# Optimization experiments

Measured on AMD Instinct MI355X. Metric: run time of the kernel, lower is better.

Reference implementation:

```python
import jax, jax.numpy as jnp
import numpy as np

K = 3  # kernel_size

def setup_inputs() -> dict:
    key = jax.random.key(0)
    k1, k2 = jax.random.split(key)
    inputs = jax.random.normal(k1, (16, 96, 96, 64), dtype=jnp.float32)
    # Dense weights for each of the K*K taps; Dense input dim == cout (conv output channels)
    W = jax.random.normal(k2, (K, K, 128, 128), dtype=jnp.float32) * 0.05
    return {"inputs": inputs, "W": W}

def reference(inputs, W):
    # inputs: [B,H,Wd,Cin], W: [K,K,cout,cout]
    B, H, Wd, Cin = inputs.shape
    pad = (K - 1) // 2  # TF 'same' padding, stride 1, odd kernel
    # One-hot conv kernel ones((cin,cout)) at tap (x,y): every output channel equals the
    # channel-sum of the zero-padded input shifted by (x-pad, y-pad).
    s = inputs.sum(axis=-1)  # [B,H,Wd]
    sp = jnp.pad(s, ((0, 0), (pad, pad), (pad, pad)))  # [B,H+2p,Wd+2p]
    # shifted[x,y,b,i,j] = sp[b, i+x, j+y]
    shifted = jnp.stack([
        jnp.stack([sp[:, x:x + H, y:y + Wd] for y in range(K)], axis=0)
        for x in range(K)], axis=0)  # [K,K,B,H,Wd]
    # Dense(no bias) on a constant-across-channels vector: out_o = s * sum_c W[c,o]
    wsum = W.sum(axis=2)  # [K,K,cout]
    out = shifted[..., None] * wsum[:, :, None, None, None, :]  # [K,K,B,H,Wd,cout]
    return out
```

## Files before the change

kernel.cpp:

```cpp
#include <hip/hip_runtime.h>

#define BQ   16
#define HH   96
#define WWD  96
#define CIN  64
#define COUT 128
#define KK   3
#define NPIX (BQ * HH * WWD)

typedef float f32x4 __attribute__((ext_vector_type(4)));

__global__ __launch_bounds__(256) void k_prep(const float* __restrict__ in,
                                              const float* __restrict__ W,
                                              float* __restrict__ s,
                                              float* __restrict__ wsum) {
    int t = threadIdx.x;
    if (blockIdx.x < KK * KK) {
        int tap = blockIdx.x;
        int o    = t & (COUT - 1);
        int half = t >> 7;
        const float* base = W + (size_t)tap * COUT * COUT + (size_t)half * 64 * COUT + o;
        float acc = 0.f;
#pragma unroll 8
        for (int c = 0; c < 64; ++c) acc += base[(size_t)c * COUT];
        __shared__ float red[256];
        red[t] = acc;
        __syncthreads();
        if (t < COUT) wsum[tap * COUT + t] = red[t] + red[t + COUT];
        return;
    }
    int pb = blockIdx.x - KK * KK;
    int g  = t & 15;
#pragma unroll
    for (int it = 0; it < 16; ++it) {
        int pixel = pb * 256 + it * 16 + (t >> 4);
        f32x4 v = __builtin_nontemporal_load(
            (const f32x4*)(in + (size_t)pixel * CIN) + g);
        float acc = (v.x + v.y) + (v.z + v.w);
        acc += __shfl_xor(acc, 1);
        acc += __shfl_xor(acc, 2);
        acc += __shfl_xor(acc, 4);
        acc += __shfl_xor(acc, 8);
        if (g == 0) s[pixel] = acc;
    }
}

__global__ __launch_bounds__(256) void k_main(const float* __restrict__ s,
                                              const float* __restrict__ wsum,
                                              float* __restrict__ out) {
    int bid = blockIdx.x;
    int tap = bid / (BQ * HH);
    int rem = bid - tap * (BQ * HH);
    int b   = rem / HH;
    int i   = rem - b * HH;
    int x   = tap / 3, y = tap - x * 3;

    int t  = threadIdx.x;
    int ob = (t & 31) * 4;
    int jt = t >> 5;

    f32x4 w = *(const f32x4*)(wsum + tap * COUT + ob);

    int ii = i + x - 1;
    bool rowok = (unsigned)ii < (unsigned)HH;
    const float* srow = s + ((size_t)b * HH + (rowok ? ii : 0)) * WWD;
    float* orow = out + (size_t)bid * (WWD * COUT) + ob;

#pragma unroll
    for (int it = 0; it < WWD / 8; ++it) {
        int j  = it * 8 + jt;
        int jj = j + y - 1;
        float sv = (rowok && (unsigned)jj < (unsigned)WWD) ? srow[jj] : 0.f;
        f32x4 v = { sv * w.x, sv * w.y, sv * w.z, sv * w.w };
        __builtin_nontemporal_store(v, (f32x4*)(orow + (size_t)j * COUT));
    }
}

extern "C" void kernel_launch(void* const* d_in, const int* in_sizes, int n_in,
                              void* d_out, int out_size, void* d_ws, size_t ws_size,
                              hipStream_t stream) {
    const float* in = (const float*)d_in[0];
    const float* W  = (const float*)d_in[1];
    float* out  = (float*)d_out;
    float* s    = (float*)d_ws;
    float* wsum = (float*)d_ws + NPIX;

    k_prep<<<KK * KK + NPIX / 256, 256, 0, stream>>>(in, W, s, wsum);
    k_main<<<KK * KK * BQ * HH, 256, 0, stream>>>(s, wsum, out);
}
```

Before: 689.7 us.

## Fuse channel-sum and weight-sum prep into the main output kernel

Removes the separate prep kernel and its workspace round trip. Each output block now sums its tap's weight columns into shared memory and computes the channel sums for its one input row into shared memory before writing the outputs. This saves a launch and the global write and re-read of the intermediate arrays. In exchange every block redoes the weight reduction and the row reduction, so weight and input reads grow by roughly the number of blocks per tap and row, mostly served from cache, and two barriers are added before the store loop.

```diff
diff --git a/kernel.cpp b/kernel.cpp
--- a/kernel.cpp
+++ b/kernel.cpp
@@ -6,48 +6,12 @@
 #define CIN  64
 #define COUT 128
 #define KK   3
-#define NPIX (BQ * HH * WWD)
 
 typedef float f32x4 __attribute__((ext_vector_type(4)));
 
-__global__ __launch_bounds__(256) void k_prep(const float* __restrict__ in,
-                                              const float* __restrict__ W,
-                                              float* __restrict__ s,
-                                              float* __restrict__ wsum) {
-    int t = threadIdx.x;
-    if (blockIdx.x < KK * KK) {
-        int tap = blockIdx.x;
-        int o    = t & (COUT - 1);
-        int half = t >> 7;
-        const float* base = W + (size_t)tap * COUT * COUT + (size_t)half * 64 * COUT + o;
-        float acc = 0.f;
-#pragma unroll 8
-        for (int c = 0; c < 64; ++c) acc += base[(size_t)c * COUT];
-        __shared__ float red[256];
-        red[t] = acc;
-        __syncthreads();
-        if (t < COUT) wsum[tap * COUT + t] = red[t] + red[t + COUT];
-        return;
-    }
-    int pb = blockIdx.x - KK * KK;
-    int g  = t & 15;
-#pragma unroll
-    for (int it = 0; it < 16; ++it) {
-        int pixel = pb * 256 + it * 16 + (t >> 4);
-        f32x4 v = __builtin_nontemporal_load(
-            (const f32x4*)(in + (size_t)pixel * CIN) + g);
-        float acc = (v.x + v.y) + (v.z + v.w);
-        acc += __shfl_xor(acc, 1);
-        acc += __shfl_xor(acc, 2);
-        acc += __shfl_xor(acc, 4);
-        acc += __shfl_xor(acc, 8);
-        if (g == 0) s[pixel] = acc;
-    }
-}
-
-__global__ __launch_bounds__(256) void k_main(const float* __restrict__ s,
-                                              const float* __restrict__ wsum,
-                                              float* __restrict__ out) {
+__global__ __launch_bounds__(256) void k_fused(const float* __restrict__ in,
+                                               const float* __restrict__ W,
+                                               float* __restrict__ out) {
     int bid = blockIdx.x;
     int tap = bid / (BQ * HH);
     int rem = bid - tap * (BQ * HH);
@@ -55,17 +19,47 @@
     int i   = rem - b * HH;
     int x   = tap / 3, y = tap - x * 3;
 
-    int t  = threadIdx.x;
-    int ob = (t & 31) * 4;
-    int jt = t >> 5;
+    int t = threadIdx.x;
 
-    f32x4 w = *(const f32x4*)(wsum + tap * COUT + ob);
+    __shared__ float ws[COUT];
+    __shared__ float srow[WWD];
+    __shared__ float red[256];
+
+    {
+        int o    = t & (COUT - 1);
+        int half = t >> 7;
+        const float* base = W + (size_t)tap * COUT * COUT + (size_t)(half * 64) * COUT + o;
+        float acc = 0.f;
+#pragma unroll 8
+        for (int c = 0; c < 64; ++c) acc += base[(size_t)c * COUT];
+        red[t] = acc;
+        __syncthreads();
+        if (t < COUT) ws[t] = red[t] + red[t + COUT];
+    }
 
     int ii = i + x - 1;
     bool rowok = (unsigned)ii < (unsigned)HH;
-    const float* srow = s + ((size_t)b * HH + (rowok ? ii : 0)) * WWD;
+    if (rowok) {
+        const float* rbase = in + ((size_t)b * HH + ii) * (WWD * CIN);
+        int g = t & 15;
+#pragma unroll
+        for (int it = 0; it < (WWD * 16) / 256; ++it) {
+            int pixel = (it * 256 + t) >> 4;
+            f32x4 v = *((const f32x4*)(rbase + (size_t)pixel * CIN) + g);
+            float acc = (v.x + v.y) + (v.z + v.w);
+            acc += __shfl_xor(acc, 1);
+            acc += __shfl_xor(acc, 2);
+            acc += __shfl_xor(acc, 4);
+            acc += __shfl_xor(acc, 8);
+            if (g == 0) srow[pixel] = acc;
+        }
+    }
+    __syncthreads();
+
+    int ob = (t & 31) * 4;
+    int jt = t >> 5;
+    f32x4 w = *(const f32x4*)(ws + ob);
     float* orow = out + (size_t)bid * (WWD * COUT) + ob;
-
 #pragma unroll
     for (int it = 0; it < WWD / 8; ++it) {
         int j  = it * 8 + jt;
@@ -81,10 +75,7 @@
                               hipStream_t stream) {
     const float* in = (const float*)d_in[0];
     const float* W  = (const float*)d_in[1];
-    float* out  = (float*)d_out;
-    float* s    = (float*)d_ws;
-    float* wsum = (float*)d_ws + NPIX;
+    float* out = (float*)d_out;
 
-    k_prep<<<KK * KK + NPIX / 256, 256, 0, stream>>>(in, W, s, wsum);
-    k_main<<<KK * KK * BQ * HH, 256, 0, stream>>>(s, wsum, out);
+    k_fused<<<KK * KK * BQ * HH, 256, 0, stream>>>(in, W, out);
 }
```

Result: no change. 699.1 us (+1.4%).
